# Performance work log

Measured on AMD Instinct MI355X. Metric: run time of the kernel, lower is better.

Reference implementation:

```python
import jax, jax.numpy as jnp
import numpy as np

N_IN, N_OUT, F, H, E, V = 80, 25, 4096, 512, 512, 4096
B = 128
BOS = V - 3  # vocab = sorted words + ['<PAD>', '<BOS>', '<EOS>', '<UNK>']
LEAK = 0.01  # torch leaky_relu default slope


def gru_cell(x, h, wih, whh, bih, bhh):
    # PyTorch GRU gate order: [r, z, n]
    gi = x @ wih.T + bih
    gh = h @ whh.T + bhh
    ir, iz, inn = jnp.split(gi, 3, axis=-1)
    hr, hz, hn = jnp.split(gh, 3, axis=-1)
    r = jax.nn.sigmoid(ir + hr)
    z = jax.nn.sigmoid(iz + hz)
    n = jnp.tanh(inn + r * hn)
    return (1.0 - z) * n + z * h


def run_gru(xs, h0, wih, whh, bih, bhh):
    # xs: [T, B, D] -> outputs [T, B, H], final hidden [B, H]
    def step(h, x):
        h2 = gru_cell(x, h, wih, whh, bih, bhh)
        return h2, h2
    hT, ys = jax.lax.scan(step, h0, xs)
    return ys, hT


def setup_inputs() -> dict:
    key = jax.random.key(0)
    ks = jax.random.split(key, 10)

    def w(k, shape, fan_in):
        return jax.random.normal(k, shape, dtype=jnp.float32) / np.float32(np.sqrt(fan_in))

    return {
        "feats": jax.random.normal(ks[0], (N_IN, B, F), dtype=jnp.float32),
        "fc_w": w(ks[1], (E, F), F),
        "fc_b": jnp.zeros((E,), jnp.float32),
        "enc_wih": w(ks[2], (3 * H, E), E),
        "enc_whh": w(ks[3], (3 * H, H), H),
        "enc_bih": jnp.zeros((3 * H,), jnp.float32),
        "enc_bhh": jnp.zeros((3 * H,), jnp.float32),
        "dec_wih": w(ks[4], (3 * H, 2 * H + E), 2 * H + E),
        "dec_whh": w(ks[5], (3 * H, H), H),
        "dec_bih": jnp.zeros((3 * H,), jnp.float32),
        "dec_bhh": jnp.zeros((3 * H,), jnp.float32),
        "out_w": w(ks[6], (V, H), H),
        "out_b": jnp.zeros((V,), jnp.float32),
        "embed": jax.random.normal(ks[7], (V, E), dtype=jnp.float32) * 0.05,
        "tgt": jax.random.randint(ks[8], (B, N_OUT), 0, V, dtype=jnp.int32),
        "tfr": 0,
    }


def reference(feats, fc_w, fc_b, enc_wih, enc_whh, enc_bih, enc_bhh,
              dec_wih, dec_whh, dec_bih, dec_bhh, out_w, out_b, embed,
              tgt, tfr):
    T_in, Bv, _ = feats.shape
    # fc + leaky_relu (dropout = identity in eval)
    xp = jax.nn.leaky_relu(feats @ fc_w.T + fc_b, LEAK)            # [T_in, B, E]
    e_seq = jnp.concatenate([xp, jnp.zeros((N_OUT, Bv, E), xp.dtype)], axis=0)
    h0 = jnp.zeros((Bv, H), xp.dtype)
    enc_out, _ = run_gru(e_seq, h0, enc_wih, enc_whh, enc_bih, enc_bhh)  # [T_in+N_OUT, B, H]
    encA = jnp.transpose(enc_out[:T_in], (1, 0, 2))                # [B, T_in, H]
    # decoder pass 1 over encoding stage: input = [zeros(H+E) ; enc_out]
    dec1_in = jnp.concatenate(
        [jnp.zeros((T_in, Bv, H + E), xp.dtype), enc_out[:T_in]], axis=-1)
    _, alpha = run_gru(dec1_in, h0, dec_wih, dec_whh, dec_bih, dec_bhh)  # [B, H]

    d0 = jnp.broadcast_to(embed[BOS], (Bv, E))                     # <BOS> embedding
    enc_tail = enc_out[T_in:T_in + N_OUT]                          # [N_OUT, B, H]
    tgt_T = tgt.T                                                  # [N_OUT, B]

    def step(carry, inp):
        h, d = carry
        et_j, t_j = inp
        # dot-product attention over the T_in encoder states (Att_ linear is unused)
        s = jnp.tanh(jnp.einsum('bih,bh->bi', encA, h))            # [B, T_in]
        w = jax.nn.softmax(s, axis=1)
        c = jnp.einsum('bi,bih->bh', w, encA)                      # [B, H]
        x = jnp.concatenate([d, et_j, c], axis=-1)                 # [B, E+2H]
        h2 = gru_cell(x, h, dec_wih, dec_whh, dec_bih, dec_bhh)
        logp = jax.nn.log_softmax(h2 @ out_w.T + out_b, axis=-1)   # [B, V]
        lj = -jnp.mean(jnp.take_along_axis(logp, t_j[:, None], axis=1))
        d_next = embed[jnp.argmax(logp, axis=-1)]                  # greedy feedback (tfr=-1)
        return (h2, d_next), lj

    _, losses = jax.lax.scan(step, (alpha, d0), (enc_tail, tgt_T))
    return jnp.sum(losses) / N_OUT
```

## Files before the change

kernel.cpp:

```cpp
#include <hip/hip_runtime.h>
#include <hip/hip_bf16.h>

#define N_OUT 25
#define BOS   4093

typedef __attribute__((ext_vector_type(8))) short bf16x8;
typedef __attribute__((ext_vector_type(4))) float f32x4;

__device__ inline unsigned short f2bf(float f) {
    unsigned int u = __builtin_bit_cast(unsigned int, f);
    unsigned int r = (u + 0x7fffu + ((u >> 16) & 1u)) >> 16;
    return (unsigned short)r;
}
__device__ inline float bf2f(unsigned short s) {
    return __builtin_bit_cast(float, (unsigned int)s << 16);
}
__device__ inline float sigf(float x) { return 1.f / (1.f + expf(-x)); }

__device__ __forceinline__ unsigned long long ld_u64_coh(const void* p) {
    return __hip_atomic_load((const unsigned long long*)p, __ATOMIC_RELAXED, __HIP_MEMORY_SCOPE_AGENT);
}
__device__ __forceinline__ void st_u64_coh(void* p, unsigned long long v) {
    __hip_atomic_store((unsigned long long*)p, v, __ATOMIC_RELAXED, __HIP_MEMORY_SCOPE_AGENT);
}
__device__ __forceinline__ void st_u32_coh(void* p, unsigned int v) {
    __hip_atomic_store((unsigned int*)p, v, __ATOMIC_RELAXED, __HIP_MEMORY_SCOPE_AGENT);
}
__device__ __forceinline__ unsigned short ld_u16_coh(const unsigned short* p) {
    return __hip_atomic_load(p, __ATOMIC_RELAXED, __HIP_MEMORY_SCOPE_AGENT);
}
__device__ __forceinline__ int ld_i32_coh(const int* p) {
    return __hip_atomic_load(p, __ATOMIC_RELAXED, __HIP_MEMORY_SCOPE_AGENT);
}
__device__ __forceinline__ void st_i32_coh(int* p, int v) {
    __hip_atomic_store(p, v, __ATOMIC_RELAXED, __HIP_MEMORY_SCOPE_AGENT);
}
__device__ inline unsigned long long pack_ff(float a, float b) {
    return ((unsigned long long)__builtin_bit_cast(unsigned int, b) << 32) |
           __builtin_bit_cast(unsigned int, a);
}
__device__ inline unsigned long long pack_if(int a, float b) {
    return ((unsigned long long)__builtin_bit_cast(unsigned int, b) << 32) |
           (unsigned int)a;
}
__device__ __forceinline__ void spin_ge(const int* p, int tgt)
{
    while (ld_i32_coh(p) < tgt) __builtin_amdgcn_s_sleep(1);
}

__device__ __forceinline__ bf16x8 ld_bf8_sc1(const unsigned short* p) {
    bf16x8 r;
    asm volatile("global_load_dwordx4 %0, %1, off sc1" : "=v"(r) : "v"(p));
    return r;
}
#define VM_FENCE do { asm volatile("s_waitcnt vmcnt(0)" ::: "memory"); \
                      __builtin_amdgcn_sched_barrier(0); } while (0)

template<int AFP32, int OUT_BF, int ACT>
__global__ __launch_bounds__(256)
void gemm_mfma(const void* __restrict__ Ap, int lda,
               const unsigned short* __restrict__ W, int ldw,
               const float* __restrict__ bias,
               void* __restrict__ Cp, int ldc, int K)
{
    __shared__ short Abuf[128 * 32];
    __shared__ short Wbuf[128 * 32];
    const int tid  = threadIdx.x;
    const int lane = tid & 63;
    const int wave = tid >> 6;
    const int wr = wave >> 1, wc = wave & 1;
    const int l15 = lane & 15, kg = lane >> 4;
    const int m0 = blockIdx.y * 128, n0 = blockIdx.x * 128;

    const float* Af = (const float*)Ap;
    const unsigned short* Ab = (const unsigned short*)Ap;

    f32x4 acc[4][4];
#pragma unroll
    for (int i = 0; i < 4; ++i)
#pragma unroll
        for (int j = 0; j < 4; ++j) acc[i][j] = f32x4{0.f, 0.f, 0.f, 0.f};

    const bf16x8* Av = (const bf16x8*)Abuf;
    const bf16x8* Wv = (const bf16x8*)Wbuf;

    for (int k0 = 0; k0 < K; k0 += 32) {
#pragma unroll
        for (int cc = 0; cc < 2; ++cc) {
            int c = tid + cc * 256;
            int row = c >> 2, k8 = (c & 3) * 8;
            if (AFP32) {
                const float* src = &Af[(size_t)(m0 + row) * lda + k0 + k8];
                float4 v0 = *reinterpret_cast<const float4*>(src);
                float4 v1 = *reinterpret_cast<const float4*>(src + 4);
                bf16x8 s;
                s[0] = (short)f2bf(v0.x); s[1] = (short)f2bf(v0.y);
                s[2] = (short)f2bf(v0.z); s[3] = (short)f2bf(v0.w);
                s[4] = (short)f2bf(v1.x); s[5] = (short)f2bf(v1.y);
                s[6] = (short)f2bf(v1.z); s[7] = (short)f2bf(v1.w);
                *reinterpret_cast<bf16x8*>(&Abuf[row * 32 + k8]) = s;
            } else {
                *reinterpret_cast<bf16x8*>(&Abuf[row * 32 + k8]) =
                    *reinterpret_cast<const bf16x8*>(&Ab[(size_t)(m0 + row) * lda + k0 + k8]);
            }
            *reinterpret_cast<bf16x8*>(&Wbuf[row * 32 + k8]) =
                *reinterpret_cast<const bf16x8*>(&W[(size_t)(n0 + row) * ldw + k0 + k8]);
        }
        __syncthreads();
        bf16x8 a[4], b[4];
#pragma unroll
        for (int i = 0; i < 4; ++i) a[i] = Av[(wr * 64 + i * 16 + l15) * 4 + kg];
#pragma unroll
        for (int j = 0; j < 4; ++j) b[j] = Wv[(wc * 64 + j * 16 + l15) * 4 + kg];
#pragma unroll
        for (int i = 0; i < 4; ++i)
#pragma unroll
            for (int j = 0; j < 4; ++j)
                acc[i][j] = __builtin_amdgcn_mfma_f32_16x16x32_bf16(a[i], b[j], acc[i][j], 0, 0, 0);
        __syncthreads();
    }

    float* Cf = (float*)Cp;
    unsigned short* Cb = (unsigned short*)Cp;
#pragma unroll
    for (int i = 0; i < 4; ++i) {
#pragma unroll
        for (int j = 0; j < 4; ++j) {
            int n = n0 + wc * 64 + j * 16 + l15;
            float bv = bias[n];
#pragma unroll
            for (int r = 0; r < 4; ++r) {
                int m = m0 + wr * 64 + i * 16 + kg * 4 + r;
                float v = acc[i][j][r] + bv;
                if (ACT == 1) v = v > 0.f ? v : 0.01f * v;
                if (OUT_BF) Cb[(size_t)m * ldc + n] = f2bf(v);
                else        Cf[(size_t)m * ldc + n] = v;
            }
        }
    }
}

__global__ __launch_bounds__(256, 1)
void recur_persist(const unsigned short* __restrict__ enc_gi_bf,
                   const float* __restrict__ enc_bih, const float* __restrict__ enc_bhh,
                   const unsigned short* __restrict__ encwhh_bf,
                   const unsigned short* __restrict__ decwih_bf,
                   const unsigned short* __restrict__ decwhh_bf,
                   const float* __restrict__ dec_bih, const float* __restrict__ dec_bhh,
                   unsigned short* __restrict__ encout_bf,
                   unsigned short* __restrict__ hDb,
                   int* efl, int* dfl)
{
    __shared__ unsigned long long tileq[512];
    unsigned short* tile16 = (unsigned short*)tileq;
    const int g = blockIdx.x;
    const int tid = threadIdx.x, w = tid >> 6, lane = tid & 63;
    const int l15 = lane & 15, kg = lane >> 4;

    if (g < 32) {
        const int cg = g >> 1, rh = g & 1;
        const int mb = rh * 64 + w * 16;
        int wrow[6];
#pragma unroll
        for (int ct = 0; ct < 6; ++ct) wrow[ct] = (ct >> 1) * 512 + cg * 32 + (ct & 1) * 16 + l15;
        float hreg[2][4] = {{0.f,0.f,0.f,0.f},{0.f,0.f,0.f,0.f}};

        for (int i = 0; i < 105; ++i) {
            if (i > 0) {
                if (tid < 32) spin_ge(&efl[tid * 32], i);
                __syncthreads();
                asm volatile("" ::: "memory");
            }
            bf16x8 areg[16];
            if (i > 0) {
                const unsigned short* ap = &encout_bf[(size_t)(i - 1) * 65536 + (size_t)(mb + l15) * 512 + kg * 8];
                VM_FENCE;
#pragma unroll
                for (int ks = 0; ks < 16; ++ks) areg[ks] = ld_bf8_sc1(ap + ks * 32);
                VM_FENCE;
            } else {
#pragma unroll
                for (int ks = 0; ks < 16; ++ks) areg[ks] = bf16x8{0,0,0,0,0,0,0,0};
            }
            f32x4 acc[6];
#pragma unroll
            for (int ct = 0; ct < 6; ++ct) acc[ct] = f32x4{0.f, 0.f, 0.f, 0.f};
#pragma unroll
            for (int ks = 0; ks < 16; ++ks) {
#pragma unroll
                for (int ct = 0; ct < 6; ++ct) {
                    bf16x8 bv = *(const bf16x8*)&encwhh_bf[(size_t)wrow[ct] * 512 + ks * 32 + kg * 8];
                    acc[ct] = __builtin_amdgcn_mfma_f32_16x16x32_bf16(areg[ks], bv, acc[ct], 0, 0, 0);
                }
            }
#pragma unroll
            for (int jh = 0; jh < 2; ++jh) {
                int jc = cg * 32 + jh * 16 + l15;
                float bhr = enc_bhh[jc], bhz = enc_bhh[512 + jc], bhn = enc_bhh[1024 + jc];
#pragma unroll
                for (int rr = 0; rr < 4; ++rr) {
                    int br = mb + kg * 4 + rr;
                    float gr_, gz_, gn_;
                    if (i < 80) {
                        const unsigned short* gp = enc_gi_bf + ((size_t)i * 128 + br) * 1536 + jc;
                        gr_ = bf2f(gp[0]); gz_ = bf2f(gp[512]); gn_ = bf2f(gp[1024]);
                    } else {
                        gr_ = enc_bih[jc]; gz_ = enc_bih[512 + jc]; gn_ = enc_bih[1024 + jc];
                    }
                    float r = sigf(gr_ + bhr + acc[jh][rr]);
                    float z = sigf(gz_ + bhz + acc[2 + jh][rr]);
                    float n = tanhf(gn_ + r * (acc[4 + jh][rr] + bhn));
                    float v = (1.f - z) * n + z * hreg[jh][rr];
                    hreg[jh][rr] = v;
                    tile16[(w * 16 + kg * 4 + rr) * 32 + jh * 16 + l15] = f2bf(v);
                }
            }
            __syncthreads();
            {
                size_t base = (size_t)i * 65536 + (size_t)(rh * 64) * 512 + cg * 32;
                int row = tid >> 3, ch = tid & 7;
                st_u64_coh(&encout_bf[base + (size_t)row * 512 + ch * 4], tileq[tid]);
                st_u64_coh(&encout_bf[base + (size_t)(32 + row) * 512 + ch * 4], tileq[256 + tid]);
            }
            __syncthreads();
            if (tid == 0) st_i32_coh(&efl[g * 32], i + 1);
        }
    } else {
        const int s = g - 32;
        const int cg = s >> 2, rq = s & 3;
        const int rt = w >> 1, cs = w & 1;
        const int mb = rq * 32 + rt * 16;
        int wrow[3];
#pragma unroll
        for (int t = 0; t < 3; ++t) wrow[t] = t * 512 + cg * 32 + cs * 16 + l15;
        const int jc = cg * 32 + cs * 16 + l15;
        float hreg[4] = {0.f, 0.f, 0.f, 0.f};

        for (int i = 1; i <= 80; ++i) {
            if (tid < 32) spin_ge(&efl[tid * 32], i);
            else if (tid >= 64 && tid < 128 && i >= 2) spin_ge(&dfl[(tid - 64) * 32], i - 1);
            __syncthreads();
            asm volatile("" ::: "memory");

            f32x4 agi[3], agh[3];
#pragma unroll
            for (int t = 0; t < 3; ++t) { agi[t] = f32x4{0.f,0.f,0.f,0.f}; agh[t] = f32x4{0.f,0.f,0.f,0.f}; }
            bf16x8 areg[16];
            {
                const unsigned short* ap = &encout_bf[(size_t)(i - 1) * 65536 + (size_t)(mb + l15) * 512 + kg * 8];
                VM_FENCE;
#pragma unroll
                for (int ks = 0; ks < 16; ++ks) areg[ks] = ld_bf8_sc1(ap + ks * 32);
                VM_FENCE;
            }
#pragma unroll
            for (int ks = 0; ks < 16; ++ks)
#pragma unroll
                for (int t = 0; t < 3; ++t) {
                    bf16x8 bv = *(const bf16x8*)&decwih_bf[(size_t)wrow[t] * 1536 + 1024 + ks * 32 + kg * 8];
                    agi[t] = __builtin_amdgcn_mfma_f32_16x16x32_bf16(areg[ks], bv, agi[t], 0, 0, 0);
                }
            if (i >= 2) {
                const unsigned short* ap = &hDb[(size_t)((i - 1) & 1) * 65536 + (size_t)(mb + l15) * 512 + kg * 8];
                VM_FENCE;
#pragma unroll
                for (int ks = 0; ks < 16; ++ks) areg[ks] = ld_bf8_sc1(ap + ks * 32);
                VM_FENCE;
            } else {
#pragma unroll
                for (int ks = 0; ks < 16; ++ks) areg[ks] = bf16x8{0,0,0,0,0,0,0,0};
            }
#pragma unroll
            for (int ks = 0; ks < 16; ++ks)
#pragma unroll
                for (int t = 0; t < 3; ++t) {
                    bf16x8 bv = *(const bf16x8*)&decwhh_bf[(size_t)wrow[t] * 512 + ks * 32 + kg * 8];
                    agh[t] = __builtin_amdgcn_mfma_f32_16x16x32_bf16(areg[ks], bv, agh[t], 0, 0, 0);
                }
            float bir = dec_bih[jc], bhr = dec_bhh[jc];
            float biz = dec_bih[512 + jc], bhz = dec_bhh[512 + jc];
            float bin_ = dec_bih[1024 + jc], bhn = dec_bhh[1024 + jc];
#pragma unroll
            for (int rr = 0; rr < 4; ++rr) {
                float r = sigf(agi[0][rr] + bir + agh[0][rr] + bhr);
                float z = sigf(agi[1][rr] + biz + agh[1][rr] + bhz);
                float n = tanhf(agi[2][rr] + bin_ + r * (agh[2][rr] + bhn));
                float v = (1.f - z) * n + z * hreg[rr];
                hreg[rr] = v;
                tile16[(rt * 16 + kg * 4 + rr) * 32 + cs * 16 + l15] = f2bf(v);
            }
            __syncthreads();
            {
                size_t base = (size_t)(i & 1) * 65536 + (size_t)(rq * 32) * 512 + cg * 32;
                int row = tid >> 3, ch = tid & 7;
                st_u64_coh(&hDb[base + (size_t)row * 512 + ch * 4], tileq[tid]);
            }
            __syncthreads();
            if (tid == 0) st_i32_coh(&dfl[s * 32], i);
        }
    }
}

__device__ void attention(int b, const unsigned short* __restrict__ hrow,
                          unsigned short* __restrict__ c_bf,
                          float* hsh, float* ssh, const unsigned short* esh)
{
    const int tid = threadIdx.x;
    if (tid < 128) {
        unsigned long long u = ld_u64_coh(&hrow[tid * 4]);
        hsh[tid * 4 + 0] = bf2f((unsigned short)(u));
        hsh[tid * 4 + 1] = bf2f((unsigned short)(u >> 16));
        hsh[tid * 4 + 2] = bf2f((unsigned short)(u >> 32));
        hsh[tid * 4 + 3] = bf2f((unsigned short)(u >> 48));
    }
    __syncthreads();
    const int wv = tid >> 6, lane = tid & 63;
    float hreg[8];
#pragma unroll
    for (int q = 0; q < 8; ++q) hreg[q] = hsh[lane * 8 + q];
#pragma unroll 4
    for (int i = wv; i < 80; i += 4) {
        bf16x8 v = *(const bf16x8*)&esh[i * 512 + lane * 8];
        float p = 0.f;
#pragma unroll
        for (int q = 0; q < 8; ++q) p += bf2f((unsigned short)v[q]) * hreg[q];
#pragma unroll
        for (int off = 32; off > 0; off >>= 1) p += __shfl_xor(p, off, 64);
        if (lane == 0) ssh[i] = tanhf(p);
    }
    __syncthreads();
    if (tid == 0) {
        float mx = -1e30f;
        for (int i = 0; i < 80; ++i) mx = fmaxf(mx, ssh[i]);
        float s = 0.f;
        for (int i = 0; i < 80; ++i) { float e = expf(ssh[i] - mx); ssh[i] = e; s += e; }
        ssh[80] = 1.0f / s;
    }
    __syncthreads();
    float acc0 = 0.f, acc1 = 0.f;
    const unsigned short* ebase = esh + tid * 2;
#pragma unroll 10
    for (int i = 0; i < 80; ++i) {
        unsigned int u = *reinterpret_cast<const unsigned int*>(&ebase[i * 512]);
        float w = ssh[i];
        acc0 += w * __builtin_bit_cast(float, u << 16);
        acc1 += w * __builtin_bit_cast(float, u & 0xffff0000u);
    }
    float inv = ssh[80];
    unsigned int packed = (unsigned int)f2bf(acc0 * inv) | ((unsigned int)f2bf(acc1 * inv) << 16);
    st_u32_coh(&c_bf[(size_t)b * 512 + tid * 2], packed);
    __syncthreads();
}

__global__ __launch_bounds__(256, 1)
void decode_persist(const unsigned short* __restrict__ encout_bf,
                    const unsigned short* __restrict__ decwih_bf, const unsigned short* __restrict__ decwhh_bf,
                    const float* __restrict__ dec_bhh,
                    const unsigned short* __restrict__ outw_bf, const float* __restrict__ out_b,
                    const unsigned short* __restrict__ emb2gi, const float* __restrict__ gie,
                    const int* __restrict__ tgt,
                    const unsigned short* __restrict__ hDb,
                    unsigned short* __restrict__ hCb,
                    unsigned short* __restrict__ c_bf,
                    unsigned long long* __restrict__ pA, unsigned long long* __restrict__ pB,
                    float* __restrict__ out,
                    int* c1, int* cp, int* c2)
{
    __shared__ unsigned short esh[80 * 512];
    __shared__ float hsh[512];
    __shared__ float ssh[88];
    __shared__ unsigned long long tileq[256];
    __shared__ float sMv[256];
    __shared__ int   sIv[256];
    __shared__ float sLv[256];
    __shared__ int   sVid[32];
    unsigned short* tile16 = (unsigned short*)tileq;

    const int g = blockIdx.x;
    const int tid = threadIdx.x, w = tid >> 6, lane = tid & 63;
    const int l15 = lane & 15, kg = lane >> 4;
    float loss_acc = 0.f;

    for (int i = w; i < 80; i += 4)
        *(bf16x8*)&esh[i * 512 + lane * 8] =
            *(const bf16x8*)&encout_bf[(size_t)i * 65536 + g * 512 + lane * 8];
    __syncthreads();

    attention(g, hDb + (size_t)g * 512, c_bf, hsh, ssh, esh);
    __syncthreads();
    if (tid == 0) st_i32_coh(&c2[g * 32], 1);

    const int cg = g >> 2, rq = g & 3;
    const int rt = w >> 1, cs = w & 1;
    const int mb = rq * 32 + rt * 16;
    const int jc = cg * 32 + cs * 16 + l15;
    int wrow[3];
#pragma unroll
    for (int t = 0; t < 3; ++t) wrow[t] = t * 512 + cg * 32 + cs * 16 + l15;
    float hreg[4] = {0.f, 0.f, 0.f, 0.f};
    if (g < 64) {
#pragma unroll
        for (int rr = 0; rr < 4; ++rr)
            hreg[rr] = bf2f(ld_u16_coh(&hDb[(size_t)(mb + kg * 4 + rr) * 512 + jc]));
    }

    for (int j = 0; j < 25; ++j) {
        const unsigned short* h_in_b = (j == 0) ? hDb : hCb + (size_t)((j - 1) & 1) * 65536;
        unsigned short* h_out_b = hCb + (size_t)(j & 1) * 65536;
        unsigned long long* pAj = pA + (size_t)(j & 1) * 16384;
        unsigned long long* pBj = pB + (size_t)(j & 1) * 16384;
        const unsigned long long* pAp = pA + (size_t)((j - 1) & 1) * 16384;
        const unsigned long long* pBp = pB + (size_t)((j - 1) & 1) * 16384;

        if (g < 64) {
            if (tid < 128) spin_ge(&c2[tid * 32], j + 1);
            else if (j >= 1) spin_ge(&cp[(tid - 128) * 32], j);
            __syncthreads();
            asm volatile("" ::: "memory");

            f32x4 agi[3], agh[3];
#pragma unroll
            for (int t = 0; t < 3; ++t) { agi[t] = f32x4{0.f,0.f,0.f,0.f}; agh[t] = f32x4{0.f,0.f,0.f,0.f}; }
            bf16x8 areg[16];

            {
                const unsigned short* ap = &c_bf[(size_t)(mb + l15) * 512 + kg * 8];
                VM_FENCE;
#pragma unroll
                for (int ks = 0; ks < 16; ++ks) areg[ks] = ld_bf8_sc1(ap + ks * 32);
                VM_FENCE;
            }
#pragma unroll
            for (int ks = 0; ks < 16; ++ks)
#pragma unroll
                for (int t = 0; t < 3; ++t) {
                    bf16x8 bv = *(const bf16x8*)&decwih_bf[(size_t)wrow[t] * 1536 + 1024 + ks * 32 + kg * 8];
                    agi[t] = __builtin_amdgcn_mfma_f32_16x16x32_bf16(areg[ks], bv, agi[t], 0, 0, 0);
                }
            {
                const unsigned short* ap = &h_in_b[(size_t)(mb + l15) * 512 + kg * 8];
                VM_FENCE;
#pragma unroll
                for (int ks = 0; ks < 16; ++ks) areg[ks] = ld_bf8_sc1(ap + ks * 32);
                VM_FENCE;
            }
#pragma unroll
            for (int ks = 0; ks < 16; ++ks)
#pragma unroll
                for (int t = 0; t < 3; ++t) {
                    bf16x8 bv = *(const bf16x8*)&decwhh_bf[(size_t)wrow[t] * 512 + ks * 32 + kg * 8];
                    agh[t] = __builtin_amdgcn_mfma_f32_16x16x32_bf16(areg[ks], bv, agh[t], 0, 0, 0);
                }

            int myvid[4];
            if (j == 0) {
#pragma unroll
                for (int rr = 0; rr < 4; ++rr) myvid[rr] = BOS;
            } else {
                const int rowl = tid >> 3, seg = tid & 7;
                const int browg = rq * 32 + rowl;
                float bm = -1e30f; int bi = 0x7fffffff;
#pragma unroll
                for (int half = 0; half < 2; ++half) {
                    unsigned long long ua[8], ub[8];
#pragma unroll
                    for (int k = 0; k < 8; ++k)
                        ua[k] = ld_u64_coh(&pAp[(size_t)browg * 128 + seg * 16 + half * 8 + k]);
#pragma unroll
                    for (int k = 0; k < 8; ++k)
                        ub[k] = ld_u64_coh(&pBp[(size_t)browg * 128 + seg * 16 + half * 8 + k]);
#pragma unroll
                    for (int k = 0; k < 8; ++k) {
                        float m = __builtin_bit_cast(float, (unsigned int)ua[k]);
                        int ii = (int)(unsigned int)ub[k];
                        if (m > bm || (m == bm && ii < bi)) { bm = m; bi = ii; }
                    }
                }
                sMv[tid] = bm; sIv[tid] = bi;
                __syncthreads();
                if (seg == 0) {
                    float m = sMv[tid]; int ii = sIv[tid];
#pragma unroll
                    for (int k = 1; k < 8; ++k) {
                        float om = sMv[tid + k]; int oi = sIv[tid + k];
                        if (om > m || (om == m && oi < ii)) { m = om; ii = oi; }
                    }
                    sVid[rowl] = ii;
                }
                __syncthreads();
#pragma unroll
                for (int rr = 0; rr < 4; ++rr) myvid[rr] = sVid[rt * 16 + kg * 4 + rr];
            }

            float bhr = dec_bhh[jc], bhz = dec_bhh[512 + jc], bhn = dec_bhh[1024 + jc];
#pragma unroll
            for (int rr = 0; rr < 4; ++rr) {
                int br = mb + kg * 4 + rr;
                const float* gp = &gie[((size_t)j * 128 + br) * 1536 + jc];
                const unsigned short* ep = &emb2gi[(size_t)myvid[rr] * 1536 + jc];
                float g0 = gp[0]    + bf2f(ep[0]);
                float g1 = gp[512]  + bf2f(ep[512]);
                float g2 = gp[1024] + bf2f(ep[1024]);
                float r = sigf(g0 + agi[0][rr] + agh[0][rr] + bhr);
                float z = sigf(g1 + agi[1][rr] + agh[1][rr] + bhz);
                float n = tanhf(g2 + agi[2][rr] + r * (agh[2][rr] + bhn));
                float v = (1.f - z) * n + z * hreg[rr];
                hreg[rr] = v;
                tile16[(rt * 16 + kg * 4 + rr) * 32 + cs * 16 + l15] = f2bf(v);
            }
            __syncthreads();
            {
                size_t base = (size_t)(j & 1) * 65536 + (size_t)(rq * 32) * 512 + cg * 32;
                int row = tid >> 3, ch = tid & 7;
                st_u64_coh(&hCb[base + (size_t)row * 512 + ch * 4], tileq[tid]);
            }
            __syncthreads();
            if (tid == 0) st_i32_coh(&c1[g * 32], j + 1);
        }

        {
            if (tid < 64) spin_ge(&c1[tid * 32], j + 1);
            __syncthreads();
            asm volatile("" ::: "memory");

            const int n0 = g * 32;
            f32x4 acc[2][2];
#pragma unroll
            for (int mt = 0; mt < 2; ++mt)
#pragma unroll
                for (int nt = 0; nt < 2; ++nt) acc[mt][nt] = f32x4{0.f,0.f,0.f,0.f};
            bf16x8 ar0[16], ar1[16];
            {
                const unsigned short* p0 = &h_out_b[(size_t)(w * 32 + l15) * 512 + kg * 8];
                const unsigned short* p1 = &h_out_b[(size_t)(w * 32 + 16 + l15) * 512 + kg * 8];
                VM_FENCE;
#pragma unroll
                for (int ks = 0; ks < 16; ++ks) ar0[ks] = ld_bf8_sc1(p0 + ks * 32);
#pragma unroll
                for (int ks = 0; ks < 16; ++ks) ar1[ks] = ld_bf8_sc1(p1 + ks * 32);
                VM_FENCE;
            }
#pragma unroll
            for (int ks = 0; ks < 16; ++ks) {
                bf16x8 b0 = *(const bf16x8*)&outw_bf[(size_t)(n0 + l15) * 512 + ks * 32 + kg * 8];
                bf16x8 b1 = *(const bf16x8*)&outw_bf[(size_t)(n0 + 16 + l15) * 512 + ks * 32 + kg * 8];
                acc[0][0] = __builtin_amdgcn_mfma_f32_16x16x32_bf16(ar0[ks], b0, acc[0][0], 0, 0, 0);
                acc[0][1] = __builtin_amdgcn_mfma_f32_16x16x32_bf16(ar0[ks], b1, acc[0][1], 0, 0, 0);
                acc[1][0] = __builtin_amdgcn_mfma_f32_16x16x32_bf16(ar1[ks], b0, acc[1][0], 0, 0, 0);
                acc[1][1] = __builtin_amdgcn_mfma_f32_16x16x32_bf16(ar1[ks], b1, acc[1][1], 0, 0, 0);
            }
            float ob0 = out_b[n0 + l15], ob1 = out_b[n0 + 16 + l15];
#pragma unroll
            for (int mt = 0; mt < 2; ++mt) {
#pragma unroll
                for (int rr = 0; rr < 4; ++rr) {
                    int m = w * 32 + mt * 16 + kg * 4 + rr;
                    float v0 = acc[mt][0][rr] + ob0;
                    float v1 = acc[mt][1][rr] + ob1;
                    int tj = tgt[m * 25 + j];
                    float pm; int pi;
                    if (v0 >= v1) { pm = v0; pi = n0 + l15; }
                    else          { pm = v1; pi = n0 + 16 + l15; }
                    float pl = -1e30f;
                    if (n0 + l15 == tj)      pl = v0;
                    if (n0 + 16 + l15 == tj) pl = v1;
#pragma unroll
                    for (int off = 1; off < 16; off <<= 1) {
                        float om = __shfl_xor(pm, off, 64);
                        int   oi = __shfl_xor(pi, off, 64);
                        float ol = __shfl_xor(pl, off, 64);
                        if (om > pm || (om == pm && oi < pi)) { pm = om; pi = oi; }
                        pl = fmaxf(pl, ol);
                    }
                    float ps = expf(v0 - pm) + expf(v1 - pm);
#pragma unroll
                    for (int off = 1; off < 16; off <<= 1) ps += __shfl_xor(ps, off, 64);
                    if (l15 == 0) {
                        st_u64_coh(&pAj[(size_t)m * 128 + g], pack_ff(pm, ps));
                        st_u64_coh(&pBj[(size_t)m * 128 + g], pack_if(pi, pl));
                    }
                }
            }
            __syncthreads();
            if (tid == 0) st_i32_coh(&cp[g * 32], j + 1);
            if (j < 24) attention(g, h_out_b + (size_t)g * 512, c_bf, hsh, ssh, esh);
            __syncthreads();
            if (tid == 0) st_i32_coh(&c2[g * 32], j + 2);
        }

        if (g >= 64) {
            if (tid < 128) spin_ge(&cp[tid * 32], j + 1);
            __syncthreads();
            asm volatile("" ::: "memory");
            const int rowb = (g - 64) * 2 + (tid >> 7);
            const int t2 = tid & 127;
            unsigned long long ua = ld_u64_coh(&pAj[(size_t)rowb * 128 + t2]);
            unsigned long long ub = ld_u64_coh(&pBj[(size_t)rowb * 128 + t2]);
            float m_ = __builtin_bit_cast(float, (unsigned int)ua);
            float s_ = __builtin_bit_cast(float, (unsigned int)(ua >> 32));
            float l_ = __builtin_bit_cast(float, (unsigned int)(ub >> 32));
            sMv[tid] = m_; sLv[tid] = l_;
            __syncthreads();
            for (int st = 64; st > 0; st >>= 1) {
                if (t2 < st) {
                    sMv[tid] = fmaxf(sMv[tid], sMv[tid + st]);
                    sLv[tid] = fmaxf(sLv[tid], sLv[tid + st]);
                }
                __syncthreads();
            }
            float M = sMv[tid & 128];
            float LT = sLv[tid & 128];
            __syncthreads();
            sMv[tid] = s_ * expf(m_ - M);
            __syncthreads();
            for (int st = 64; st > 0; st >>= 1) {
                if (t2 < st) sMv[tid] += sMv[tid + st];
                __syncthreads();
            }
            if (t2 == 0) loss_acc += -(LT - (M + logf(sMv[tid])));
            __syncthreads();
        }
    }

    if (g >= 64 && (tid == 0 || tid == 128))
        atomicAdd(out, loss_acc * (1.0f / 3200.0f));
}

__global__ void cast_f2b(const float* __restrict__ in, unsigned short* __restrict__ out, int n)
{
    int i = (blockIdx.x * 256 + threadIdx.x) * 4;
    if (i < n) {
        float4 v = *reinterpret_cast<const float4*>(&in[i]);
        out[i + 0] = f2bf(v.x); out[i + 1] = f2bf(v.y);
        out[i + 2] = f2bf(v.z); out[i + 3] = f2bf(v.w);
    }
}

extern "C" void kernel_launch(void* const* d_in, const int* in_sizes, int n_in,
                              void* d_out, int out_size, void* d_ws, size_t ws_size,
                              hipStream_t stream)
{
    const float* feats   = (const float*)d_in[0];
    const float* fc_w    = (const float*)d_in[1];
    const float* fc_b    = (const float*)d_in[2];
    const float* enc_wih = (const float*)d_in[3];
    const float* enc_whh = (const float*)d_in[4];
    const float* enc_bih = (const float*)d_in[5];
    const float* enc_bhh = (const float*)d_in[6];
    const float* dec_wih = (const float*)d_in[7];
    const float* dec_whh = (const float*)d_in[8];
    const float* dec_bih = (const float*)d_in[9];
    const float* dec_bhh = (const float*)d_in[10];
    const float* out_w   = (const float*)d_in[11];
    const float* out_b   = (const float*)d_in[12];
    const float* embed   = (const float*)d_in[13];
    const int*   tgt     = (const int*)d_in[14];

    float* ws = (float*)d_ws;
    size_t off = 0;
    auto afl = [&](size_t n) { float* r = ws + off; off += n; return r; };

    unsigned short* enc_gi_bf = (unsigned short*)afl(7864320);
    unsigned short* encout_bf = (unsigned short*)afl(3440640);
    unsigned short* xp_bf     = (unsigned short*)afl(2621440);
    unsigned short* fcw_bf    = (unsigned short*)afl(1048576);
    unsigned short* encwih_bf = (unsigned short*)afl(393216);
    unsigned short* encwhh_bf = (unsigned short*)afl(393216);
    unsigned short* decwih_bf = (unsigned short*)afl(1179648);
    unsigned short* decwhh_bf = (unsigned short*)afl(393216);
    unsigned short* outw_bf   = (unsigned short*)afl(1048576);
    unsigned short* embed_bf  = (unsigned short*)afl(1048576);
    unsigned short* emb2gi    = (unsigned short*)afl(3145728);
    float* gie               = afl(4915200);
    float* zbias             = afl(1536);
    unsigned short* hDb       = (unsigned short*)afl(65536);
    unsigned short* hCb       = (unsigned short*)afl(65536);
    unsigned short* c_bf      = (unsigned short*)afl(32768);
    unsigned long long* pA   = (unsigned long long*)afl(65536);
    unsigned long long* pB   = (unsigned long long*)afl(65536);
    int* flags               = (int*)afl(16384);

    int* efl = flags;
    int* dfl = flags + 32 * 32;
    int* c1  = flags + 96 * 32;
    int* cp  = flags + 160 * 32;
    int* c2  = flags + 288 * 32;

    hipMemsetAsync(zbias, 0, 1536 * sizeof(float), stream);
    hipMemsetAsync(flags, 0, 16384 * sizeof(int), stream);
    hipMemsetAsync(d_out, 0, sizeof(float), stream);

    cast_f2b<<<2048, 256, 0, stream>>>(fc_w, fcw_bf, 2097152);
    cast_f2b<<<768, 256, 0, stream>>>(enc_wih, encwih_bf, 786432);
    cast_f2b<<<768, 256, 0, stream>>>(enc_whh, encwhh_bf, 786432);
    cast_f2b<<<2304, 256, 0, stream>>>(dec_wih, decwih_bf, 2359296);
    cast_f2b<<<768, 256, 0, stream>>>(dec_whh, decwhh_bf, 786432);
    cast_f2b<<<2048, 256, 0, stream>>>(out_w, outw_bf, 2097152);
    cast_f2b<<<2048, 256, 0, stream>>>(embed, embed_bf, 2097152);

    gemm_mfma<1, 1, 1><<<dim3(4, 80), 256, 0, stream>>>(feats, 4096, fcw_bf, 4096, fc_b, xp_bf, 512, 4096);
    gemm_mfma<0, 1, 0><<<dim3(12, 80), 256, 0, stream>>>(xp_bf, 512, encwih_bf, 512, enc_bih, enc_gi_bf, 1536, 512);
    gemm_mfma<0, 1, 0><<<dim3(12, 32), 256, 0, stream>>>(embed_bf, 512, decwih_bf, 1536, zbias, emb2gi, 1536, 512);

    recur_persist<<<96, 256, 0, stream>>>(enc_gi_bf, enc_bih, enc_bhh, encwhh_bf,
                                          decwih_bf, decwhh_bf, dec_bih, dec_bhh,
                                          encout_bf, hDb, efl, dfl);

    gemm_mfma<0, 0, 0><<<dim3(12, 25), 256, 0, stream>>>(encout_bf + (size_t)80 * 65536, 512,
                                                         decwih_bf + 512, 1536, dec_bih, gie, 1536, 512);

    decode_persist<<<128, 256, 0, stream>>>(encout_bf, decwih_bf, decwhh_bf,
                                            dec_bhh, outw_bf, out_b,
                                            emb2gi, gie, tgt,
                                            hDb, hCb, c_bf, pA, pB, (float*)d_out,
                                            c1, cp, c2);
}
```

Measured before the change: 3.450 ms.

## Repartition persistent GRU recurrence by batch row groups to localize flag dependencies

```diff
diff --git a/kernel.cpp b/kernel.cpp
--- a/kernel.cpp
+++ b/kernel.cpp
@@ -151,55 +151,62 @@
                    unsigned short* __restrict__ hDb,
                    int* efl, int* dfl)
 {
-    __shared__ unsigned long long tileq[512];
-    unsigned short* tile16 = (unsigned short*)tileq;
+    __shared__ unsigned short hA[16 * 520];
+    __shared__ unsigned short hB[16 * 520];
+    __shared__ unsigned short tp[16 * 132];
+
     const int g = blockIdx.x;
     const int tid = threadIdx.x, w = tid >> 6, lane = tid & 63;
     const int l15 = lane & 15, kg = lane >> 4;
+    const int srow = tid >> 4, sseg = tid & 15;
 
     if (g < 32) {
-        const int cg = g >> 1, rh = g & 1;
-        const int mb = rh * 64 + w * 16;
+        const int r = g >> 2, c = g & 3;
+        const int R0 = r * 16;
+        const int hc0 = c * 128 + w * 32;
         int wrow[6];
 #pragma unroll
-        for (int ct = 0; ct < 6; ++ct) wrow[ct] = (ct >> 1) * 512 + cg * 32 + (ct & 1) * 16 + l15;
+        for (int a = 0; a < 6; ++a) wrow[a] = (a >> 1) * 512 + hc0 + (a & 1) * 16 + l15;
         float hreg[2][4] = {{0.f,0.f,0.f,0.f},{0.f,0.f,0.f,0.f}};
 
         for (int i = 0; i < 105; ++i) {
+            f32x4 acc[6];
+#pragma unroll
+            for (int a = 0; a < 6; ++a) acc[a] = f32x4{0.f,0.f,0.f,0.f};
+
             if (i > 0) {
-                if (tid < 32) spin_ge(&efl[tid * 32], i);
+                if (tid < 4) spin_ge(&efl[(r * 4 + tid) * 32], i);
                 __syncthreads();
                 asm volatile("" ::: "memory");
-            }
-            bf16x8 areg[16];
-            if (i > 0) {
-                const unsigned short* ap = &encout_bf[(size_t)(i - 1) * 65536 + (size_t)(mb + l15) * 512 + kg * 8];
+                const unsigned short* src = encout_bf + (size_t)(i - 1) * 65536
+                                          + (size_t)(R0 + srow) * 512 + sseg * 32;
+                bf16x8 ld[4];
                 VM_FENCE;
 #pragma unroll
-                for (int ks = 0; ks < 16; ++ks) areg[ks] = ld_bf8_sc1(ap + ks * 32);
+                for (int k = 0; k < 4; ++k) ld[k] = ld_bf8_sc1(src + k * 8);
                 VM_FENCE;
-            } else {
-#pragma unroll
-                for (int ks = 0; ks < 16; ++ks) areg[ks] = bf16x8{0,0,0,0,0,0,0,0};
-            }
-            f32x4 acc[6];
-#pragma unroll
-            for (int ct = 0; ct < 6; ++ct) acc[ct] = f32x4{0.f, 0.f, 0.f, 0.f};
-#pragma unroll
-            for (int ks = 0; ks < 16; ++ks) {
-#pragma unroll
-                for (int ct = 0; ct < 6; ++ct) {
-                    bf16x8 bv = *(const bf16x8*)&encwhh_bf[(size_t)wrow[ct] * 512 + ks * 32 + kg * 8];
-                    acc[ct] = __builtin_amdgcn_mfma_f32_16x16x32_bf16(areg[ks], bv, acc[ct], 0, 0, 0);
-                }
-            }
-#pragma unroll
-            for (int jh = 0; jh < 2; ++jh) {
-                int jc = cg * 32 + jh * 16 + l15;
+#pragma unroll
+                for (int k = 0; k < 4; ++k)
+                    *(bf16x8*)&hA[srow * 520 + sseg * 32 + k * 8] = ld[k];
+                __syncthreads();
+#pragma unroll
+                for (int ks = 0; ks < 16; ++ks) {
+                    bf16x8 a = *(const bf16x8*)&hA[l15 * 520 + ks * 32 + kg * 8];
+#pragma unroll
+                    for (int t = 0; t < 6; ++t) {
+                        bf16x8 bv = *(const bf16x8*)&encwhh_bf[(size_t)wrow[t] * 512 + ks * 32 + kg * 8];
+                        acc[t] = __builtin_amdgcn_mfma_f32_16x16x32_bf16(a, bv, acc[t], 0, 0, 0);
+                    }
+                }
+                __syncthreads();
+            }
+#pragma unroll
+            for (int ct = 0; ct < 2; ++ct) {
+                int jc = hc0 + ct * 16 + l15;
                 float bhr = enc_bhh[jc], bhz = enc_bhh[512 + jc], bhn = enc_bhh[1024 + jc];
 #pragma unroll
                 for (int rr = 0; rr < 4; ++rr) {
-                    int br = mb + kg * 4 + rr;
+                    int br = R0 + kg * 4 + rr;
                     float gr_, gz_, gn_;
                     if (i < 80) {
                         const unsigned short* gp = enc_gi_bf + ((size_t)i * 128 + br) * 1536 + jc;
@@ -207,96 +214,115 @@
                     } else {
                         gr_ = enc_bih[jc]; gz_ = enc_bih[512 + jc]; gn_ = enc_bih[1024 + jc];
                     }
-                    float r = sigf(gr_ + bhr + acc[jh][rr]);
-                    float z = sigf(gz_ + bhz + acc[2 + jh][rr]);
-                    float n = tanhf(gn_ + r * (acc[4 + jh][rr] + bhn));
-                    float v = (1.f - z) * n + z * hreg[jh][rr];
-                    hreg[jh][rr] = v;
-                    tile16[(w * 16 + kg * 4 + rr) * 32 + jh * 16 + l15] = f2bf(v);
-                }
-            }
-            __syncthreads();
-            {
-                size_t base = (size_t)i * 65536 + (size_t)(rh * 64) * 512 + cg * 32;
-                int row = tid >> 3, ch = tid & 7;
-                st_u64_coh(&encout_bf[base + (size_t)row * 512 + ch * 4], tileq[tid]);
-                st_u64_coh(&encout_bf[base + (size_t)(32 + row) * 512 + ch * 4], tileq[256 + tid]);
+                    float rv = sigf(gr_ + bhr + acc[ct][rr]);
+                    float zv = sigf(gz_ + bhz + acc[2 + ct][rr]);
+                    float nv = tanhf(gn_ + rv * (acc[4 + ct][rr] + bhn));
+                    float v = (1.f - zv) * nv + zv * hreg[ct][rr];
+                    hreg[ct][rr] = v;
+                    tp[(kg * 4 + rr) * 132 + w * 32 + ct * 16 + l15] = f2bf(v);
+                }
+            }
+            __syncthreads();
+#pragma unroll
+            for (int rep = 0; rep < 2; ++rep) {
+                int idx = tid + rep * 256;
+                int row = idx >> 5, q = idx & 31;
+                unsigned long long v = *(const unsigned long long*)&tp[row * 132 + q * 4];
+                st_u64_coh(&encout_bf[(size_t)i * 65536 + (size_t)(R0 + row) * 512 + c * 128 + q * 4], v);
             }
             __syncthreads();
             if (tid == 0) st_i32_coh(&efl[g * 32], i + 1);
         }
     } else {
-        const int s = g - 32;
-        const int cg = s >> 2, rq = s & 3;
-        const int rt = w >> 1, cs = w & 1;
-        const int mb = rq * 32 + rt * 16;
-        int wrow[3];
-#pragma unroll
-        for (int t = 0; t < 3; ++t) wrow[t] = t * 512 + cg * 32 + cs * 16 + l15;
-        const int jc = cg * 32 + cs * 16 + l15;
-        float hreg[4] = {0.f, 0.f, 0.f, 0.f};
+        const int g2 = g - 32;
+        const int r = g2 >> 2, c = g2 & 3;
+        const int R0 = r * 16;
+        const int hc0 = c * 128 + w * 32;
+        int wrow[6];
+#pragma unroll
+        for (int a = 0; a < 6; ++a) wrow[a] = (a >> 1) * 512 + hc0 + (a & 1) * 16 + l15;
+        float hreg[2][4] = {{0.f,0.f,0.f,0.f},{0.f,0.f,0.f,0.f}};
 
         for (int i = 1; i <= 80; ++i) {
-            if (tid < 32) spin_ge(&efl[tid * 32], i);
-            else if (tid >= 64 && tid < 128 && i >= 2) spin_ge(&dfl[(tid - 64) * 32], i - 1);
+            if (tid < 4) spin_ge(&efl[(r * 4 + tid) * 32], i);
+            else if (tid >= 4 && tid < 8 && i >= 2) spin_ge(&dfl[(r * 4 + tid - 4) * 32], i - 1);
             __syncthreads();
             asm volatile("" ::: "memory");
 
-            f32x4 agi[3], agh[3];
-#pragma unroll
-            for (int t = 0; t < 3; ++t) { agi[t] = f32x4{0.f,0.f,0.f,0.f}; agh[t] = f32x4{0.f,0.f,0.f,0.f}; }
-            bf16x8 areg[16];
-            {
-                const unsigned short* ap = &encout_bf[(size_t)(i - 1) * 65536 + (size_t)(mb + l15) * 512 + kg * 8];
-                VM_FENCE;
-#pragma unroll
-                for (int ks = 0; ks < 16; ++ks) areg[ks] = ld_bf8_sc1(ap + ks * 32);
-                VM_FENCE;
-            }
-#pragma unroll
-            for (int ks = 0; ks < 16; ++ks)
-#pragma unroll
-                for (int t = 0; t < 3; ++t) {
+            bf16x8 ldA[4], ldB[4];
+            const unsigned short* srcA = encout_bf + (size_t)(i - 1) * 65536
+                                       + (size_t)(R0 + srow) * 512 + sseg * 32;
+            VM_FENCE;
+#pragma unroll
+            for (int k = 0; k < 4; ++k) ldA[k] = ld_bf8_sc1(srcA + k * 8);
+            if (i >= 2) {
+                const unsigned short* srcB = hDb + (size_t)((i - 1) & 1) * 65536
+                                           + (size_t)(R0 + srow) * 512 + sseg * 32;
+#pragma unroll
+                for (int k = 0; k < 4; ++k) ldB[k] = ld_bf8_sc1(srcB + k * 8);
+            }
+            VM_FENCE;
+#pragma unroll
+            for (int k = 0; k < 4; ++k)
+                *(bf16x8*)&hA[srow * 520 + sseg * 32 + k * 8] = ldA[k];
+            if (i >= 2) {
+#pragma unroll
+                for (int k = 0; k < 4; ++k)
+                    *(bf16x8*)&hB[srow * 520 + sseg * 32 + k * 8] = ldB[k];
+            }
+            __syncthreads();
+
+            f32x4 agi[6], agh[6];
+#pragma unroll
+            for (int t = 0; t < 6; ++t) { agi[t] = f32x4{0.f,0.f,0.f,0.f}; agh[t] = f32x4{0.f,0.f,0.f,0.f}; }
+#pragma unroll
+            for (int ks = 0; ks < 16; ++ks) {
+                bf16x8 a = *(const bf16x8*)&hA[l15 * 520 + ks * 32 + kg * 8];
+#pragma unroll
+                for (int t = 0; t < 6; ++t) {
                     bf16x8 bv = *(const bf16x8*)&decwih_bf[(size_t)wrow[t] * 1536 + 1024 + ks * 32 + kg * 8];
-                    agi[t] = __builtin_amdgcn_mfma_f32_16x16x32_bf16(areg[ks], bv, agi[t], 0, 0, 0);
-                }
+                    agi[t] = __builtin_amdgcn_mfma_f32_16x16x32_bf16(a, bv, agi[t], 0, 0, 0);
+                }
+            }
             if (i >= 2) {
-                const unsigned short* ap = &hDb[(size_t)((i - 1) & 1) * 65536 + (size_t)(mb + l15) * 512 + kg * 8];
-                VM_FENCE;
-#pragma unroll
-                for (int ks = 0; ks < 16; ++ks) areg[ks] = ld_bf8_sc1(ap + ks * 32);
-                VM_FENCE;
-            } else {
-#pragma unroll
-                for (int ks = 0; ks < 16; ++ks) areg[ks] = bf16x8{0,0,0,0,0,0,0,0};
-            }
-#pragma unroll
-            for (int ks = 0; ks < 16; ++ks)
-#pragma unroll
-                for (int t = 0; t < 3; ++t) {
-                    bf16x8 bv = *(const bf16x8*)&decwhh_bf[(size_t)wrow[t] * 512 + ks * 32 + kg * 8];
-                    agh[t] = __builtin_amdgcn_mfma_f32_16x16x32_bf16(areg[ks], bv, agh[t], 0, 0, 0);
-                }
-            float bir = dec_bih[jc], bhr = dec_bhh[jc];
-            float biz = dec_bih[512 + jc], bhz = dec_bhh[512 + jc];
-            float bin_ = dec_bih[1024 + jc], bhn = dec_bhh[1024 + jc];
-#pragma unroll
-            for (int rr = 0; rr < 4; ++rr) {
-                float r = sigf(agi[0][rr] + bir + agh[0][rr] + bhr);
-                float z = sigf(agi[1][rr] + biz + agh[1][rr] + bhz);
-                float n = tanhf(agi[2][rr] + bin_ + r * (agh[2][rr] + bhn));
-                float v = (1.f - z) * n + z * hreg[rr];
-                hreg[rr] = v;
-                tile16[(rt * 16 + kg * 4 + rr) * 32 + cs * 16 + l15] = f2bf(v);
-            }
-            __syncthreads();
-            {
-                size_t base = (size_t)(i & 1) * 65536 + (size_t)(rq * 32) * 512 + cg * 32;
-                int row = tid >> 3, ch = tid & 7;
-                st_u64_coh(&hDb[base + (size_t)row * 512 + ch * 4], tileq[tid]);
-            }
-            __syncthreads();
-            if (tid == 0) st_i32_coh(&dfl[s * 32], i);
+#pragma unroll
+                for (int ks = 0; ks < 16; ++ks) {
+                    bf16x8 a = *(const bf16x8*)&hB[l15 * 520 + ks * 32 + kg * 8];
+#pragma unroll
+                    for (int t = 0; t < 6; ++t) {
+                        bf16x8 bv = *(const bf16x8*)&decwhh_bf[(size_t)wrow[t] * 512 + ks * 32 + kg * 8];
+                        agh[t] = __builtin_amdgcn_mfma_f32_16x16x32_bf16(a, bv, agh[t], 0, 0, 0);
+                    }
+                }
+            }
+            __syncthreads();
+
+#pragma unroll
+            for (int ct = 0; ct < 2; ++ct) {
+                int jc = hc0 + ct * 16 + l15;
+                float bir = dec_bih[jc], bhr = dec_bhh[jc];
+                float biz = dec_bih[512 + jc], bhz = dec_bhh[512 + jc];
+                float bin_ = dec_bih[1024 + jc], bhn = dec_bhh[1024 + jc];
+#pragma unroll
+                for (int rr = 0; rr < 4; ++rr) {
+                    float rv = sigf(agi[ct][rr] + bir + agh[ct][rr] + bhr);
+                    float zv = sigf(agi[2 + ct][rr] + biz + agh[2 + ct][rr] + bhz);
+                    float nv = tanhf(agi[4 + ct][rr] + bin_ + rv * (agh[4 + ct][rr] + bhn));
+                    float v = (1.f - zv) * nv + zv * hreg[ct][rr];
+                    hreg[ct][rr] = v;
+                    tp[(kg * 4 + rr) * 132 + w * 32 + ct * 16 + l15] = f2bf(v);
+                }
+            }
+            __syncthreads();
+#pragma unroll
+            for (int rep = 0; rep < 2; ++rep) {
+                int idx = tid + rep * 256;
+                int row = idx >> 5, q = idx & 31;
+                unsigned long long v = *(const unsigned long long*)&tp[row * 132 + q * 4];
+                st_u64_coh(&hDb[(size_t)(i & 1) * 65536 + (size_t)(R0 + row) * 512 + c * 128 + q * 4], v);
+            }
+            __syncthreads();
+            if (tid == 0) st_i32_coh(&dfl[g2 * 32], i);
         }
     }
 }
@@ -702,7 +728,7 @@
     gemm_mfma<0, 1, 0><<<dim3(12, 80), 256, 0, stream>>>(xp_bf, 512, encwih_bf, 512, enc_bih, enc_gi_bf, 1536, 512);
     gemm_mfma<0, 1, 0><<<dim3(12, 32), 256, 0, stream>>>(embed_bf, 512, decwih_bf, 1536, zbias, emb2gi, 1536, 512);
 
-    recur_persist<<<96, 256, 0, stream>>>(enc_gi_bf, enc_bih, enc_bhh, encwhh_bf,
+    recur_persist<<<64, 256, 0, stream>>>(enc_gi_bf, enc_bih, enc_bhh, encwhh_bf,
                                           decwih_bf, decwhh_bf, dec_bih, dec_bhh,
                                           encout_bf, hDb, efl, dfl);
 
```

After: 3.822 ms. 1.11x slower.

## Reorder decoder step to run attention before vocab projection and merge cast kernels

Applied to the files above, without the earlier changes.

```diff
diff --git a/kernel.cpp b/kernel.cpp
--- a/kernel.cpp
+++ b/kernel.cpp
@@ -405,7 +405,6 @@
     }
 
     for (int j = 0; j < 25; ++j) {
-        const unsigned short* h_in_b = (j == 0) ? hDb : hCb + (size_t)((j - 1) & 1) * 65536;
         unsigned short* h_out_b = hCb + (size_t)(j & 1) * 65536;
         unsigned long long* pAj = pA + (size_t)(j & 1) * 16384;
         unsigned long long* pBj = pB + (size_t)(j & 1) * 16384;
@@ -413,8 +412,8 @@
         const unsigned long long* pBp = pB + (size_t)((j - 1) & 1) * 16384;
 
         if (g < 64) {
+            const unsigned short* h_in_b = (j == 0) ? hDb : hCb + (size_t)((j - 1) & 1) * 65536;
             if (tid < 128) spin_ge(&c2[tid * 32], j + 1);
-            else if (j >= 1) spin_ge(&cp[(tid - 128) * 32], j);
             __syncthreads();
             asm volatile("" ::: "memory");
 
@@ -457,6 +456,9 @@
 #pragma unroll
                 for (int rr = 0; rr < 4; ++rr) myvid[rr] = BOS;
             } else {
+                if (tid < 128) spin_ge(&cp[tid * 32], j);
+                __syncthreads();
+                asm volatile("" ::: "memory");
                 const int rowl = tid >> 3, seg = tid & 7;
                 const int browg = rq * 32 + rowl;
                 float bm = -1e30f; int bi = 0x7fffffff;
@@ -523,6 +525,10 @@
             __syncthreads();
             asm volatile("" ::: "memory");
 
+            if (j < 24) attention(g, h_out_b + (size_t)g * 512, c_bf, hsh, ssh, esh);
+            __syncthreads();
+            if (tid == 0) st_i32_coh(&c2[g * 32], j + 2);
+
             const int n0 = g * 32;
             f32x4 acc[2][2];
 #pragma unroll
@@ -583,9 +589,6 @@
             }
             __syncthreads();
             if (tid == 0) st_i32_coh(&cp[g * 32], j + 1);
-            if (j < 24) attention(g, h_out_b + (size_t)g * 512, c_bf, hsh, ssh, esh);
-            __syncthreads();
-            if (tid == 0) st_i32_coh(&c2[g * 32], j + 2);
         }
 
         if (g >= 64) {
@@ -626,14 +629,30 @@
         atomicAdd(out, loss_acc * (1.0f / 3200.0f));
 }
 
-__global__ void cast_f2b(const float* __restrict__ in, unsigned short* __restrict__ out, int n)
+__global__ __launch_bounds__(256)
+void cast_all(const float* __restrict__ fc_w, const float* __restrict__ enc_wih,
+              const float* __restrict__ enc_whh, const float* __restrict__ dec_wih,
+              const float* __restrict__ dec_whh, const float* __restrict__ out_w,
+              const float* __restrict__ embed,
+              unsigned short* __restrict__ d_fcw, unsigned short* __restrict__ d_encwih,
+              unsigned short* __restrict__ d_encwhh, unsigned short* __restrict__ d_decwih,
+              unsigned short* __restrict__ d_decwhh, unsigned short* __restrict__ d_outw,
+              unsigned short* __restrict__ d_embed)
 {
-    int i = (blockIdx.x * 256 + threadIdx.x) * 4;
-    if (i < n) {
-        float4 v = *reinterpret_cast<const float4*>(&in[i]);
-        out[i + 0] = f2bf(v.x); out[i + 1] = f2bf(v.y);
-        out[i + 2] = f2bf(v.z); out[i + 3] = f2bf(v.w);
-    }
+    long i = (long)(blockIdx.x * 256 + threadIdx.x) * 4;
+    const float* s; unsigned short* d; long off;
+    if      (i <  2097152) { s = fc_w;    d = d_fcw;    off = 0; }
+    else if (i <  2883584) { s = enc_wih; d = d_encwih; off = 2097152; }
+    else if (i <  3670016) { s = enc_whh; d = d_encwhh; off = 2883584; }
+    else if (i <  6029312) { s = dec_wih; d = d_decwih; off = 3670016; }
+    else if (i <  6815744) { s = dec_whh; d = d_decwhh; off = 6029312; }
+    else if (i <  8912896) { s = out_w;   d = d_outw;   off = 6815744; }
+    else if (i < 11010048) { s = embed;   d = d_embed;  off = 8912896; }
+    else return;
+    i -= off;
+    float4 v = *reinterpret_cast<const float4*>(&s[i]);
+    d[i + 0] = f2bf(v.x); d[i + 1] = f2bf(v.y);
+    d[i + 2] = f2bf(v.z); d[i + 3] = f2bf(v.w);
 }
 
 extern "C" void kernel_launch(void* const* d_in, const int* in_sizes, int n_in,
@@ -690,13 +709,9 @@
     hipMemsetAsync(flags, 0, 16384 * sizeof(int), stream);
     hipMemsetAsync(d_out, 0, sizeof(float), stream);
 
-    cast_f2b<<<2048, 256, 0, stream>>>(fc_w, fcw_bf, 2097152);
-    cast_f2b<<<768, 256, 0, stream>>>(enc_wih, encwih_bf, 786432);
-    cast_f2b<<<768, 256, 0, stream>>>(enc_whh, encwhh_bf, 786432);
-    cast_f2b<<<2304, 256, 0, stream>>>(dec_wih, decwih_bf, 2359296);
-    cast_f2b<<<768, 256, 0, stream>>>(dec_whh, decwhh_bf, 786432);
-    cast_f2b<<<2048, 256, 0, stream>>>(out_w, outw_bf, 2097152);
-    cast_f2b<<<2048, 256, 0, stream>>>(embed, embed_bf, 2097152);
+    cast_all<<<10752, 256, 0, stream>>>(fc_w, enc_wih, enc_whh, dec_wih, dec_whh, out_w, embed,
+                                        fcw_bf, encwih_bf, encwhh_bf, decwih_bf, decwhh_bf,
+                                        outw_bf, embed_bf);
 
     gemm_mfma<1, 1, 1><<<dim3(4, 80), 256, 0, stream>>>(feats, 4096, fcw_bf, 4096, fc_b, xp_bf, 512, 4096);
     gemm_mfma<0, 1, 0><<<dim3(12, 80), 256, 0, stream>>>(xp_bf, 512, encwih_bf, 512, enc_bih, enc_gi_bf, 1536, 512);
```

Result: no change. 3.385 ms (-1.9%).
